# Optimization experiments

Measured on AMD Instinct MI355X. Metric: run time of the kernel, lower is better.

Reference implementation:

```python
import jax, jax.numpy as jnp
import numpy as np

D_MODEL = 1024
DEPTH = 1024

def setup_inputs() -> dict:
    key = jax.random.key(0)
    ks = jax.random.split(key, 7)
    scale = 1.0 / np.sqrt(D_MODEL)
    x = jax.random.normal(ks[0], (4, 2048, D_MODEL), dtype=jnp.float32)
    Wq = jax.random.normal(ks[1], (D_MODEL, DEPTH), dtype=jnp.float32) * scale
    Wk = jax.random.normal(ks[2], (D_MODEL, DEPTH), dtype=jnp.float32) * scale
    Wv = jax.random.normal(ks[3], (D_MODEL, DEPTH), dtype=jnp.float32) * scale
    bq = jnp.zeros((DEPTH,), dtype=jnp.float32)
    bk = jnp.zeros((DEPTH,), dtype=jnp.float32)
    bv = jnp.zeros((DEPTH,), dtype=jnp.float32)
    return {"x": x, "Wq": Wq, "bq": bq, "Wk": Wk, "bk": bk, "Wv": Wv, "bv": bv}

def reference(x, Wq, bq, Wk, bk, Wv, bv):
    # Q/K/V linear projections (Keras Dense: x @ W + b)
    q = jnp.einsum('bsd,de->bse', x, Wq) + bq  # [B,S,depth]
    k = jnp.einsum('bsd,de->bse', x, Wk) + bk
    v = jnp.einsum('bsd,de->bse', x, Wv) + bv
    d_k = jnp.asarray(q.shape[-1], dtype=q.dtype)
    scores = jnp.einsum('bse,bte->bst', q, k) / jnp.sqrt(d_k)  # [B,S,S]
    attn = jax.nn.softmax(scores, axis=-1)
    return jnp.einsum('bst,bte->bse', attn, v)  # [B,S,depth]
```

## Files before the change

kernel.cpp:

```cpp
#include <hip/hip_runtime.h>
#include <stdint.h>
#include <type_traits>

typedef unsigned short u16;
using short8  = __attribute__((ext_vector_type(8))) short;
using floatx4 = __attribute__((ext_vector_type(4))) float;

#define IC(n) (std::integral_constant<int, (n)>())

__device__ __forceinline__ u16 f2bf(float f) {
    unsigned u = __float_as_uint(f);
    u += 0x7fff + ((u >> 16) & 1);
    return (u16)(u >> 16);
}
__device__ __forceinline__ float bf2f(u16 h) {
    return __uint_as_float(((unsigned)h) << 16);
}

__device__ __forceinline__ void gload_lds16(const void* g, void* l) {
    auto gp = reinterpret_cast<const __attribute__((address_space(1))) unsigned int*>(
        reinterpret_cast<uintptr_t>(g));
    auto lp = reinterpret_cast<__attribute__((address_space(3))) unsigned int*>(
        reinterpret_cast<uintptr_t>(l));
    __builtin_amdgcn_global_load_lds(gp, lp, 16, 0, 0);
}

__global__ __launch_bounds__(256) void cvt_f32_bf16_kernel(
        const float* __restrict__ in, u16* __restrict__ out) {
    long i = ((long)blockIdx.x * 256 + threadIdx.x) * 4;
    float4 v = *(const float4*)(in + i);
    ushort4 o;
    o.x = f2bf(v.x); o.y = f2bf(v.y); o.z = f2bf(v.z); o.w = f2bf(v.w);
    *(ushort4*)(out + i) = o;
}

__global__ __launch_bounds__(256) void wt_kernel(
        const float* __restrict__ W0, const float* __restrict__ W1, const float* __restrict__ W2,
        u16* __restrict__ O0, u16* __restrict__ O1, u16* __restrict__ O2) {
    const float* W = blockIdx.z == 0 ? W0 : blockIdx.z == 1 ? W1 : W2;
    u16* O = blockIdx.z == 0 ? O0 : blockIdx.z == 1 ? O1 : O2;
    __shared__ float t[32][33];
    const int cx = threadIdx.x & 31, ry = threadIdx.x >> 5;
    const int d0 = blockIdx.x * 32, e0 = blockIdx.y * 32;
#pragma unroll
    for (int i = 0; i < 4; i++) t[ry + i * 8][cx] = W[(long)(d0 + ry + i * 8) * 1024 + e0 + cx];
    __syncthreads();
#pragma unroll
    for (int i = 0; i < 4; i++) O[(long)(e0 + ry + i * 8) * 1024 + d0 + cx] = f2bf(t[cx][ry + i * 8]);
}

__global__ __launch_bounds__(256) void vt_kernel(
        const u16* __restrict__ V, u16* __restrict__ Vt) {
    const int b = blockIdx.z;
    const u16* v = V + (long)b * 2048 * 1024;
    u16* o = Vt + (long)b * 1024 * 2048;
    __shared__ u16 t[64][68];
    const int c4 = (threadIdx.x & 15) * 4, r = threadIdx.x >> 4;
    const int e0 = blockIdx.x * 64, t0 = blockIdx.y * 64;
#pragma unroll
    for (int i = 0; i < 4; i++)
        *(ushort4*)&t[r + i * 16][c4] =
            *(const ushort4*)(v + (long)(t0 + r + i * 16) * 1024 + e0 + c4);
    __syncthreads();
#pragma unroll
    for (int i = 0; i < 4; i++) {
        const int e = r + i * 16;
        ushort4 d;
        d.x = t[c4 + 0][e]; d.y = t[c4 + 1][e]; d.z = t[c4 + 2][e]; d.w = t[c4 + 3][e];
        *(ushort4*)(o + (long)(e0 + e) * 2048 + t0 + c4) = d;
    }
}

template <int MODE, int BNT>
__global__ __launch_bounds__(512) void gemm8_kernel(
        const u16* __restrict__ A, const u16* __restrict__ Bt,
        void* __restrict__ out0, void* __restrict__ out1, void* __restrict__ out2,
        const float* __restrict__ b0, const float* __restrict__ b1, const float* __restrict__ b2,
        int K, int N, long sAb, long sBb, long sCb, float scale)
{
    extern __shared__ u16 lds[];
    constexpr int DB   = (BNT == 256) ? 32768 : 24576;
    constexpr int FNH  = (BNT == 256) ? 2 : 1;
    constexpr int WCOL = (BNT == 256) ? 64 : 32;
    const int tid = threadIdx.x, lane = tid & 63, wid = tid >> 6;
    const int wm = wid >> 2, wn = wid & 3;
    const int l15 = lane & 15, hib = (lane >> 4) * 16;

    const int nbx = gridDim.x;
    const int nwg = nbx * gridDim.y;
    int lin = blockIdx.y * nbx + blockIdx.x;
    lin = (lin & 7) * (nwg >> 3) + (lin >> 3);
    const long m0 = (long)(lin / nbx) * 256;
    const long n0 = (long)(lin % nbx) * BNT;

    const u16* Ab = A + (long)blockIdx.z * sAb;
    const u16* Bb = Bt + (long)blockIdx.z * sBb;
    const long ldk = K;
    const int NT = K >> 6;

    auto stA = [&](int dbuf, int S, int kt) {
#pragma unroll
        for (int i = 0; i < 2; ++i) {
            const int rl = tid >> 3;
            const int R  = S * 64 + rl;
            const int cb = (tid & 7) * 16;
            const int scb = cb ^ ((R & 7) << 4);
            const u16* src = Ab + (m0 + i * 128 + R) * ldk + (long)kt * 64 + (scb >> 1);
            u16* dst = lds + dbuf * DB + i * 8192 + S * 4096 + wid * 512;
            gload_lds16(src, dst);
        }
    };
    auto stB = [&](int dbuf, int NHs, int kt) {
#pragma unroll
        for (int i = 0; i < 2; ++i) {
            const int c = i * 2 + (wid >> 2);
            const int h = c >> 1, rb = (c & 1) * 64;
            const int w = (wid & 3) * 64 + lane;
            const int r32 = w >> 3;
            const int R = rb + NHs * 32 + r32;
            const int cb = (w & 7) * 16;
            const int scb = cb ^ ((R & 7) << 4);
            const u16* src = Bb + (n0 + h * 128 + R) * ldk + (long)kt * 64 + (scb >> 1);
            u16* dst = lds + dbuf * DB + 16384 + h * 8192 + (rb + NHs * 32) * 64 + (wid & 3) * 512;
            gload_lds16(src, dst);
        }
    };
    auto stB128 = [&](int dbuf, int kt) {
#pragma unroll
        for (int i = 0; i < 2; ++i) {
            const int R = i * 64 + (tid >> 3);
            const int cb = (tid & 7) * 16;
            const int scb = cb ^ ((R & 7) << 4);
            const u16* src = Bb + (n0 + R) * ldk + (long)kt * 64 + (scb >> 1);
            u16* dst = lds + dbuf * DB + 16384 + i * 4096 + tid * 8;
            gload_lds16(src, dst);
        }
    };

    floatx4 acc[8][2 * FNH] = {};
    short8 afr[4][2], bfr[FNH][2];

    auto LA = [&](int dbuf, auto MHc) {
        constexpr int MH = decltype(MHc)::value;
        const char* reg = (const char*)(lds + dbuf * DB + wm * 8192);
#pragma unroll
        for (int fm = 0; fm < 4; ++fm)
#pragma unroll
            for (int ks = 0; ks < 2; ++ks) {
                const int r = MH * 64 + fm * 16 + l15;
                const int cb = ks * 64 + hib;
                afr[fm][ks] = *(const short8*)(reg + r * 128 + (cb ^ ((r & 7) << 4)));
            }
    };
    auto LB = [&](int dbuf, auto NHc) {
        constexpr int NH = decltype(NHc)::value;
        if constexpr (BNT == 256) {
            const char* reg = (const char*)(lds + dbuf * DB + 16384 + (wn >> 1) * 8192);
#pragma unroll
            for (int fn = 0; fn < 2; ++fn)
#pragma unroll
                for (int ks = 0; ks < 2; ++ks) {
                    const int r = (wn & 1) * 64 + NH * 32 + fn * 16 + l15;
                    const int cb = ks * 64 + hib;
                    bfr[fn][ks] = *(const short8*)(reg + r * 128 + (cb ^ ((r & 7) << 4)));
                }
        } else {
            const char* reg = (const char*)(lds + dbuf * DB + 16384);
#pragma unroll
            for (int ks = 0; ks < 2; ++ks) {
                const int r = wn * 32 + NH * 16 + l15;
                const int cb = ks * 64 + hib;
                bfr[0][ks] = *(const short8*)(reg + r * 128 + (cb ^ ((r & 7) << 4)));
            }
        }
    };
    auto MM = [&](auto MHc, auto NHc) {
        constexpr int MH = decltype(MHc)::value;
        constexpr int NH = decltype(NHc)::value;
        __builtin_amdgcn_s_setprio(1);
#pragma unroll
        for (int fm = 0; fm < 4; ++fm)
#pragma unroll
            for (int fn = 0; fn < FNH; ++fn)
#pragma unroll
                for (int ks = 0; ks < 2; ++ks)
                    acc[MH * 4 + fm][NH * FNH + fn] = __builtin_amdgcn_mfma_f32_16x16x32_bf16(
                        afr[fm][ks], bfr[fn][ks], acc[MH * 4 + fm][NH * FNH + fn], 0, 0, 0);
        __builtin_amdgcn_s_setprio(0);
    };

#define BAR() __builtin_amdgcn_s_barrier()

    if constexpr (BNT == 256) {
        stA(0, 0, 0); stA(0, 1, 0); stB(0, 0, 0); stB(0, 1, 0);
        stA(1, 0, 1); stB(1, 1, 1);
        asm volatile("s_waitcnt vmcnt(4)");
    } else {
        stA(0, 0, 0); stA(0, 1, 0); stB128(0, 0);
        stA(1, 0, 1);
        asm volatile("s_waitcnt vmcnt(2)");
    }
    BAR();

    auto pair = [&](auto LASTC, int kt0) {
        constexpr bool L = decltype(LASTC)::value;
        if constexpr (BNT == 256) {
            stA(1, 1, kt0 + 1); stB(1, 0, kt0 + 1);
            LA(0, IC(0)); LB(0, IC(0));
            BAR();
            MM(IC(0), IC(0));
            LB(0, IC(1));
            MM(IC(0), IC(1));
            LA(0, IC(1));
            BAR();
            if (!L) { stA(0, 0, kt0 + 2); stB(0, 1, kt0 + 2); }
            BAR();
            MM(IC(1), IC(1));
            LB(0, IC(0));
            MM(IC(1), IC(0));
            if (L) asm volatile("s_waitcnt vmcnt(0)");
            else   asm volatile("s_waitcnt vmcnt(4)");
            BAR();
            if (!L) { stA(0, 1, kt0 + 2); stB(0, 0, kt0 + 2); }
            LA(1, IC(0)); LB(1, IC(0));
            BAR();
            MM(IC(0), IC(0));
            LB(1, IC(1));
            MM(IC(0), IC(1));
            LA(1, IC(1));
            BAR();
            if (!L) { stA(1, 0, kt0 + 3); stB(1, 1, kt0 + 3); }
            BAR();
            MM(IC(1), IC(1));
            LB(1, IC(0));
            MM(IC(1), IC(0));
            if (L) asm volatile("s_waitcnt vmcnt(0)");
            else   asm volatile("s_waitcnt vmcnt(4)");
            BAR();
        } else {
            stA(1, 1, kt0 + 1); stB128(1, kt0 + 1);
            LA(0, IC(0)); LB(0, IC(0));
            BAR();
            MM(IC(0), IC(0));
            LB(0, IC(1));
            MM(IC(0), IC(1));
            LA(0, IC(1));
            BAR();
            if (!L) stA(0, 0, kt0 + 2);
            BAR();
            MM(IC(1), IC(1));
            LB(0, IC(0));
            MM(IC(1), IC(0));
            if (L) asm volatile("s_waitcnt vmcnt(0)");
            else   asm volatile("s_waitcnt vmcnt(2)");
            BAR();
            if (!L) { stA(0, 1, kt0 + 2); stB128(0, kt0 + 2); }
            LA(1, IC(0)); LB(1, IC(0));
            BAR();
            MM(IC(0), IC(0));
            LB(1, IC(1));
            MM(IC(0), IC(1));
            LA(1, IC(1));
            BAR();
            if (!L) stA(1, 0, kt0 + 3);
            BAR();
            MM(IC(1), IC(1));
            LB(1, IC(0));
            MM(IC(1), IC(0));
            if (L) asm volatile("s_waitcnt vmcnt(0)");
            else   asm volatile("s_waitcnt vmcnt(2)");
            BAR();
        }
    };

    const int NITER = NT >> 1;
    int it = 0;
    for (; it < NITER - 1; ++it) pair(std::false_type{}, 2 * it);
    pair(std::true_type{}, 2 * it);

#undef BAR

    const int cr = (lane >> 4) * 4, cc = l15;
    if (MODE == 0) {
        const int sel = (int)(n0 >> 10);
        u16* O = (u16*)(sel == 0 ? out0 : sel == 1 ? out1 : out2);
        const float* bias = sel == 0 ? b0 : sel == 1 ? b1 : b2;
        const long nc0 = n0 & 1023;
#pragma unroll
        for (int an = 0; an < 2 * FNH; ++an) {
            const long col = nc0 + wn * WCOL + an * 16 + cc;
            const float bvv = bias[col];
#pragma unroll
            for (int am = 0; am < 8; ++am) {
                const long row = m0 + wm * 128 + am * 16 + cr;
#pragma unroll
                for (int j = 0; j < 4; ++j)
                    O[(row + j) * 1024 + col] = f2bf(acc[am][an][j] + bvv);
            }
        }
    } else {
#pragma unroll
        for (int an = 0; an < 2 * FNH; ++an) {
            const long col = n0 + wn * WCOL + an * 16 + cc;
#pragma unroll
            for (int am = 0; am < 8; ++am) {
                const long row = m0 + wm * 128 + am * 16 + cr;
#pragma unroll
                for (int j = 0; j < 4; ++j) {
                    const long idx = (long)blockIdx.z * sCb + (row + j) * (long)N + col;
                    if (MODE == 1) ((u16*)out0)[idx] = f2bf(acc[am][an][j] * scale);
                    else           ((float*)out0)[idx] = acc[am][an][j];
                }
            }
        }
    }
}

__global__ __launch_bounds__(256) void softmax_kernel(u16* __restrict__ S) {
    u16* p = S + (long)blockIdx.x * 2048;
    const int tid = threadIdx.x;
    union { int4 q; u16 u[8]; } in;
    in.q = *(const int4*)(p + tid * 8);
    float v[8];
#pragma unroll
    for (int i = 0; i < 8; i++) v[i] = bf2f(in.u[i]);
    float mx = v[0];
#pragma unroll
    for (int i = 1; i < 8; i++) mx = fmaxf(mx, v[i]);
#pragma unroll
    for (int off = 32; off; off >>= 1) mx = fmaxf(mx, __shfl_xor(mx, off));
    __shared__ float red[8];
    if ((tid & 63) == 0) red[tid >> 6] = mx;
    __syncthreads();
    mx = fmaxf(fmaxf(red[0], red[1]), fmaxf(red[2], red[3]));
    float s = 0.f;
#pragma unroll
    for (int i = 0; i < 8; i++) { v[i] = __expf(v[i] - mx); s += v[i]; }
#pragma unroll
    for (int off = 32; off; off >>= 1) s += __shfl_xor(s, off);
    if ((tid & 63) == 0) red[4 + (tid >> 6)] = s;
    __syncthreads();
    s = red[4] + red[5] + red[6] + red[7];
    const float inv = 1.f / s;
    union { int4 q; u16 u[8]; } out;
#pragma unroll
    for (int i = 0; i < 8; i++) out.u[i] = f2bf(v[i] * inv);
    *(int4*)(p + tid * 8) = out.q;
}

extern "C" void kernel_launch(void* const* d_in, const int* in_sizes, int n_in,
                              void* d_out, int out_size, void* d_ws, size_t ws_size,
                              hipStream_t stream) {
    const float* x  = (const float*)d_in[0];
    const float* Wq = (const float*)d_in[1];
    const float* bq = (const float*)d_in[2];
    const float* Wk = (const float*)d_in[3];
    const float* bk = (const float*)d_in[4];
    const float* Wv = (const float*)d_in[5];
    const float* bv = (const float*)d_in[6];
    float* out = (float*)d_out;

    char* ws = (char*)d_ws;
    const long MB = 1L << 20;
    u16* xb = (u16*)(ws);
    u16* wt = (u16*)(ws + 16 * MB);
    u16* Q  = (u16*)(ws + 22 * MB);
    u16* Kb = (u16*)(ws + 38 * MB);
    u16* Vb = (u16*)(ws + 54 * MB);
    u16* Vt = (u16*)(ws + 70 * MB);
    u16* Sc = (u16*)(ws + 86 * MB);

    (void)hipFuncSetAttribute((const void*)gemm8_kernel<0, 256>, hipFuncAttributeMaxDynamicSharedMemorySize, 131072);
    (void)hipFuncSetAttribute((const void*)gemm8_kernel<1, 256>, hipFuncAttributeMaxDynamicSharedMemorySize, 131072);
    (void)hipFuncSetAttribute((const void*)gemm8_kernel<2, 128>, hipFuncAttributeMaxDynamicSharedMemorySize, 131072);

    cvt_f32_bf16_kernel<<<8192, 256, 0, stream>>>(x, xb);
    wt_kernel<<<dim3(32, 32, 3), 256, 0, stream>>>(Wq, Wk, Wv, wt, wt + 1024 * 1024, wt + 2 * 1024 * 1024);
    gemm8_kernel<0, 256><<<dim3(12, 32, 1), 512, 131072, stream>>>(
        xb, wt, Q, Kb, Vb, bq, bk, bv, 1024, 3072, 0, 0, 0, 1.f);
    vt_kernel<<<dim3(16, 32, 4), 256, 0, stream>>>(Vb, Vt);
    gemm8_kernel<1, 256><<<dim3(8, 8, 4), 512, 131072, stream>>>(
        Q, Kb, Sc, nullptr, nullptr, nullptr, nullptr, nullptr,
        1024, 2048, 2048L * 1024, 2048L * 1024, 2048L * 2048, 0.03125f);
    softmax_kernel<<<8192, 256, 0, stream>>>(Sc);
    gemm8_kernel<2, 128><<<dim3(8, 8, 4), 512, 98304, stream>>>(
        Sc, Vt, out, nullptr, nullptr, nullptr, nullptr, nullptr,
        2048, 1024, 2048L * 2048, 1024L * 2048, 2048L * 1024, 1.f);
}
```

Baseline: 183.1 us.

## Stage GEMM epilogue through LDS for vectorized stores, retile QKV projection

The GEMM epilogue now writes accumulators into swizzled LDS first. It then reads them back as 16-byte vectors and issues coalesced global stores, replacing scattered 2- and 4-byte stores. The QKV projection moves from 256-wide to 128-wide N tiles with twice as many blocks, and the PV GEMM gets enough dynamic LDS to stage its fp32 tile. The MFMA loop order is also swapped so the k-step is outermost. In exchange, each block pays extra syncthreads and an LDS round trip at the end.

After: 180.9 us. No clear change (-1.2%).

```diff
diff --git a/kernel.cpp b/kernel.cpp
--- a/kernel.cpp
+++ b/kernel.cpp
@@ -4,6 +4,7 @@
 
 typedef unsigned short u16;
 using short8  = __attribute__((ext_vector_type(8))) short;
+using ushort8 = __attribute__((ext_vector_type(8))) unsigned short;
 using floatx4 = __attribute__((ext_vector_type(4))) float;
 
 #define IC(n) (std::integral_constant<int, (n)>())
@@ -179,11 +180,11 @@
         constexpr int NH = decltype(NHc)::value;
         __builtin_amdgcn_s_setprio(1);
 #pragma unroll
-        for (int fm = 0; fm < 4; ++fm)
-#pragma unroll
-            for (int fn = 0; fn < FNH; ++fn)
-#pragma unroll
-                for (int ks = 0; ks < 2; ++ks)
+        for (int ks = 0; ks < 2; ++ks)
+#pragma unroll
+            for (int fm = 0; fm < 4; ++fm)
+#pragma unroll
+                for (int fn = 0; fn < FNH; ++fn)
                     acc[MH * 4 + fm][NH * FNH + fn] = __builtin_amdgcn_mfma_f32_16x16x32_bf16(
                         afr[fm][ks], bfr[fn][ks], acc[MH * 4 + fm][NH * FNH + fn], 0, 0, 0);
         __builtin_amdgcn_s_setprio(0);
@@ -281,36 +282,67 @@
 #undef BAR
 
     const int cr = (lane >> 4) * 4, cc = l15;
-    if (MODE == 0) {
-        const int sel = (int)(n0 >> 10);
-        u16* O = (u16*)(sel == 0 ? out0 : sel == 1 ? out1 : out2);
-        const float* bias = sel == 0 ? b0 : sel == 1 ? b1 : b2;
+    char* ldsB = (char*)lds;
+    __syncthreads();
+    if (MODE == 2) {
+#pragma unroll
+        for (int an = 0; an < 2 * FNH; ++an) {
+            const int col = wn * WCOL + an * 16 + cc;
+#pragma unroll
+            for (int am = 0; am < 8; ++am) {
+                const int row = wm * 128 + am * 16 + cr;
+#pragma unroll
+                for (int j = 0; j < 4; ++j)
+                    *(float*)(ldsB + ((((row + j) * BNT + col) * 4) ^ (((row + j) & 7) << 4))) =
+                        acc[am][an][j];
+            }
+        }
+        __syncthreads();
+        constexpr int NIT = 256 * BNT / 4 / 512;
+        float* O = (float*)out0 + (long)blockIdx.z * sCb;
+#pragma unroll
+        for (int i = 0; i < NIT; ++i) {
+            const int g4 = tid + i * 512;
+            const int row = g4 >> 5;
+            const int c4  = g4 & 31;
+            float4 v = *(const float4*)(ldsB + ((g4 * 16) ^ ((row & 7) << 4)));
+            *(float4*)(O + (m0 + row) * (long)N + n0 + c4 * 4) = v;
+        }
+    } else {
+        const int sel = (MODE == 0) ? (int)(n0 >> 10) : 0;
+        const float* bias = (MODE == 0) ? (sel == 0 ? b0 : sel == 1 ? b1 : b2) : nullptr;
         const long nc0 = n0 & 1023;
 #pragma unroll
         for (int an = 0; an < 2 * FNH; ++an) {
-            const long col = nc0 + wn * WCOL + an * 16 + cc;
-            const float bvv = bias[col];
+            const int col = wn * WCOL + an * 16 + cc;
+            const float bvv = (MODE == 0) ? bias[nc0 + col] : 0.f;
 #pragma unroll
             for (int am = 0; am < 8; ++am) {
-                const long row = m0 + wm * 128 + am * 16 + cr;
-#pragma unroll
-                for (int j = 0; j < 4; ++j)
-                    O[(row + j) * 1024 + col] = f2bf(acc[am][an][j] + bvv);
+                const int row = wm * 128 + am * 16 + cr;
+#pragma unroll
+                for (int j = 0; j < 4; ++j) {
+                    float v = acc[am][an][j];
+                    if (MODE == 1) v *= scale;
+                    v += bvv;
+                    *(u16*)(ldsB + ((((row + j) * BNT + col) * 2) ^ (((row + j) & 7) << 4))) = f2bf(v);
+                }
             }
         }
-    } else {
-#pragma unroll
-        for (int an = 0; an < 2 * FNH; ++an) {
-            const long col = n0 + wn * WCOL + an * 16 + cc;
-#pragma unroll
-            for (int am = 0; am < 8; ++am) {
-                const long row = m0 + wm * 128 + am * 16 + cr;
-#pragma unroll
-                for (int j = 0; j < 4; ++j) {
-                    const long idx = (long)blockIdx.z * sCb + (row + j) * (long)N + col;
-                    if (MODE == 1) ((u16*)out0)[idx] = f2bf(acc[am][an][j] * scale);
-                    else           ((float*)out0)[idx] = acc[am][an][j];
-                }
+        __syncthreads();
+        constexpr int NIT = 256 * BNT / 8 / 512;
+        constexpr int RSH = (BNT == 256) ? 5 : 4;
+#pragma unroll
+        for (int i = 0; i < NIT; ++i) {
+            const int g8 = tid + i * 512;
+            const int row = g8 >> RSH;
+            const int c8  = g8 & ((BNT >> 3) - 1);
+            ushort8 v = *(const ushort8*)(ldsB + ((g8 * 16) ^ ((row & 7) << 4)));
+            if (MODE == 0) {
+                u16* O = (u16*)(sel == 0 ? out0 : sel == 1 ? out1 : out2);
+                *(ushort8*)(O + (m0 + row) * 1024 + nc0 + c8 * 8) = v;
+            } else {
+                u16* O = (u16*)out0 + (long)blockIdx.z * sCb;
+                *(ushort8*)(O + (m0 + row) * (long)N + n0 + c8 * 8) = v;
             }
         }
     }
@@ -370,20 +402,20 @@
     u16* Vt = (u16*)(ws + 70 * MB);
     u16* Sc = (u16*)(ws + 86 * MB);
 
-    (void)hipFuncSetAttribute((const void*)gemm8_kernel<0, 256>, hipFuncAttributeMaxDynamicSharedMemorySize, 131072);
+    (void)hipFuncSetAttribute((const void*)gemm8_kernel<0, 128>, hipFuncAttributeMaxDynamicSharedMemorySize, 131072);
     (void)hipFuncSetAttribute((const void*)gemm8_kernel<1, 256>, hipFuncAttributeMaxDynamicSharedMemorySize, 131072);
     (void)hipFuncSetAttribute((const void*)gemm8_kernel<2, 128>, hipFuncAttributeMaxDynamicSharedMemorySize, 131072);
 
     cvt_f32_bf16_kernel<<<8192, 256, 0, stream>>>(x, xb);
     wt_kernel<<<dim3(32, 32, 3), 256, 0, stream>>>(Wq, Wk, Wv, wt, wt + 1024 * 1024, wt + 2 * 1024 * 1024);
-    gemm8_kernel<0, 256><<<dim3(12, 32, 1), 512, 131072, stream>>>(
+    gemm8_kernel<0, 128><<<dim3(24, 32, 1), 512, 98304, stream>>>(
         xb, wt, Q, Kb, Vb, bq, bk, bv, 1024, 3072, 0, 0, 0, 1.f);
     vt_kernel<<<dim3(16, 32, 4), 256, 0, stream>>>(Vb, Vt);
     gemm8_kernel<1, 256><<<dim3(8, 8, 4), 512, 131072, stream>>>(
         Q, Kb, Sc, nullptr, nullptr, nullptr, nullptr, nullptr,
         1024, 2048, 2048L * 1024, 2048L * 1024, 2048L * 2048, 0.03125f);
     softmax_kernel<<<8192, 256, 0, stream>>>(Sc);
-    gemm8_kernel<2, 128><<<dim3(8, 8, 4), 512, 98304, stream>>>(
+    gemm8_kernel<2, 128><<<dim3(8, 8, 4), 512, 131072, stream>>>(
         Sc, Vt, out, nullptr, nullptr, nullptr, nullptr, nullptr,
         2048, 1024, 2048L * 2048, 1024L * 2048, 2048L * 1024, 1.f);
 }
```
